# Kernel tuning notes

Measured on AMD Instinct MI355X. Metric: run time of the kernel, lower is better.

## Reference

```python
import jax, jax.numpy as jnp
import numpy as np
from jax import lax

K = 5        # kernel_size
KN = 32      # kernel_num
C_IN = 16
PRIOR_VAR = 0.01


def _extract_patches(x, k):
    # TF tf.image.extract_patches VALID, stride 1: last-dim order is (kh, kw, c)
    B, H, W, C = x.shape
    Ho, Wo = H - k + 1, W - k + 1
    p = jnp.stack([x[:, i:i + Ho, j:j + Wo, :] for i in range(k) for j in range(k)], axis=3)
    return p.reshape(B, Ho * Wo, k * k * C)  # [B, P, k*k*C]


def setup_inputs() -> dict:
    key = jax.random.key(0)
    k1, k2, k3, k4 = jax.random.split(key, 4)
    mu_in = jax.random.normal(k1, (32, 64, 64, C_IN), dtype=jnp.float32)
    Sigma_in = jax.random.uniform(k2, (32, 64, 64, C_IN), dtype=jnp.float32)
    # GlorotNormal for w_mu
    fan_in = K * K * C_IN
    fan_out = K * K * KN
    std = jnp.sqrt(2.0 / (fan_in + fan_out)).astype(jnp.float32)
    w_mu = jax.random.normal(k3, (K, K, C_IN, KN), dtype=jnp.float32) * std
    w_sigma = jax.random.uniform(k4, (KN,), dtype=jnp.float32, minval=-4.6, maxval=-2.25)
    return {"mu_in": mu_in, "Sigma_in": Sigma_in, "w_mu": w_mu, "w_sigma": w_sigma}


def reference(mu_in, Sigma_in, w_mu, w_sigma):
    B = mu_in.shape[0]
    # KL regularizer (broadcast w_sigma over w_mu shape, mean over all)
    kl_loss = (jnp.log(PRIOR_VAR) - 1.0 - w_sigma
               + jax.nn.softplus(w_sigma) / PRIOR_VAR
               + jnp.square(w_mu) / PRIOR_VAR)
    kl_conv = 0.5 * jnp.mean(kl_loss)

    w_sigma_2 = jax.nn.softplus(w_sigma)  # [KN]

    # mean path: standard conv
    mu_out = lax.conv_general_dilated(
        mu_in, w_mu, window_strides=(1, 1), padding='VALID',
        dimension_numbers=('NHWC', 'HWIO', 'NHWC'))  # [B, Ho, Wo, KN]
    Ho = mu_out.shape[1]

    mu_dim = jnp.float32(K * K * C_IN)

    diag_sigma_g = _extract_patches(Sigma_in, K)          # [B, P, D]
    mu_in_patches = _extract_patches(mu_in, K)            # [B, P, D]

    mu_cov_square = jnp.square(w_mu).reshape(K * K * C_IN, KN)
    mu_wT_sigmags_mu_w = diag_sigma_g @ (mu_cov_square / mu_dim)          # [B, P, KN]
    trace = jnp.sum(diag_sigma_g, axis=2, keepdims=True) * w_sigma_2 / mu_dim  # [B, P, KN]
    mu_gT_mu_g = jnp.sum(jnp.square(mu_in_patches), axis=-1, keepdims=True)    # [B, P, 1]
    sigmaw_mu_gT_mu_g = mu_gT_mu_g * w_sigma_2 / mu_dim                   # [B, P, KN]

    Sigma_out = trace + mu_wT_sigmags_mu_w + sigmaw_mu_gT_mu_g
    Sigma_out = jax.nn.softplus(Sigma_out.reshape(B, Ho, Ho, KN))
    return mu_out, Sigma_out, kl_conv
```

## Files before the change

kernel.cpp:

```cpp
#include <hip/hip_runtime.h>
#include <hip/hip_bf16.h>
#include <math.h>

#define KK 5
#define KN 32
#define CIN 16
#define H 64
#define W 64
#define NB 32
#define HO 60
#define WO 60
#define D_TOT 400
#define OUT_PLANE (NB*HO*WO*KN)

#define TH 8
#define TW 16
#define IN_R 12
#define IN_C 20
#define CPAD 24
#define TILE_SH (IN_R*IN_C*CPAD)
#define NKSTEP 13

typedef short short8 __attribute__((ext_vector_type(8)));
typedef float f32x4 __attribute__((ext_vector_type(4)));

__device__ ushort g_bmu[13312];
__device__ ushort g_bsq[13312];
__device__ float  g_spw[32];

__device__ __forceinline__ ushort f2bf(float x) {
    __hip_bfloat16 h = __float2bfloat16(x);
    return *reinterpret_cast<ushort*>(&h);
}
__device__ __forceinline__ float bf2f(ushort u) {
    __hip_bfloat16 h = *reinterpret_cast<__hip_bfloat16*>(&u);
    return __bfloat162float(h);
}
__device__ __forceinline__ float softplusf(float x) {
    return (x > 20.0f) ? x : __logf(1.0f + __expf(x));
}

__global__ void prep_all(const float* __restrict__ w_mu, const float* __restrict__ w_sigma,
                         float* __restrict__ kl_out) {
    __shared__ float red[256];
    int t = threadIdx.x;
    if (blockIdx.x < 52) {
        int idx = blockIdx.x * 256 + t;
        int j  = idx & 7;
        int l  = (idx >> 3) & 63;
        int nt = (idx >> 9) & 1;
        int ts = idx >> 10;
        int k  = ts * 32 + ((l >> 4) & 3) * 8 + j;
        int n  = nt * 16 + (l & 15);
        float w = (k < D_TOT) ? w_mu[k * KN + n] : 0.0f;
        g_bmu[idx] = f2bf(w);
        g_bsq[idx] = f2bf(w * w * (1.0f / 400.0f));
    } else {
        float s = 0.f;
        for (int i = t; i < D_TOT * KN; i += 256) { float w = w_mu[i]; s += w * w; }
        red[t] = s;
        __syncthreads();
        for (int off = 128; off > 0; off >>= 1) {
            if (t < off) red[t] += red[t + off];
            __syncthreads();
        }
        float sum_w2 = red[0];
        if (t < KN) {
            float ws = w_sigma[t];
            g_spw[t] = log1pf(expf(ws)) * (1.0f / 400.0f);
        }
        if (t == 0) {
            float sws = 0.f;
            for (int kn = 0; kn < KN; ++kn) {
                float ws = w_sigma[kn];
                float sp = log1pf(expf(ws));
                sws += -ws + sp * 100.0f;
            }
            float kl = 0.5f * (-4.605170186f - 1.0f + sws * (1.0f / 32.0f)
                               + sum_w2 * (100.0f / 12800.0f));
            *kl_out = kl;
        }
    }
}

__global__ __launch_bounds__(256, 4)
void vdp_main(const float* __restrict__ mu_in, const float* __restrict__ sig_in,
              float* __restrict__ mu_out, float* __restrict__ sig_out) {
    __shared__ ushort tiles[2 * TILE_SH + 8];
    __shared__ float csum[IN_R * IN_C];
    __shared__ float t12s[TH * TW];

    const int b   = blockIdx.z;
    const int ho0 = blockIdx.y * TH;
    const int wo0 = blockIdx.x * TW;
    const int t   = threadIdx.x;

    if (t < 8) tiles[2 * TILE_SH + t] = 0;

    for (int i = t; i < IN_R * IN_C * 4; i += 256) {
        int row = i / 80;
        int rem = i - row * 80;
        int col = rem >> 2, c4 = rem & 3;
        int gh = ho0 + row, gw = wo0 + col;
        float4 vm = make_float4(0.f, 0.f, 0.f, 0.f), vs = vm;
        if (gh < H && gw < W) {
            size_t g = (((size_t)b * H + gh) * W + gw) * CIN + c4 * 4;
            vm = *(const float4*)(mu_in + g);
            vs = *(const float4*)(sig_in + g);
        }
        int sb = (row * IN_C + col) * CPAD + c4 * 4;
        ushort4 um, us;
        um.x = f2bf(vm.x); um.y = f2bf(vm.y); um.z = f2bf(vm.z); um.w = f2bf(vm.w);
        us.x = f2bf(vs.x); us.y = f2bf(vs.y); us.z = f2bf(vs.z); us.w = f2bf(vs.w);
        *(ushort4*)&tiles[sb] = um;
        *(ushort4*)&tiles[TILE_SH + sb] = us;
    }
    __syncthreads();

    if (t < IN_R * IN_C) {
        int sb = t * CPAD;
        float acc = 0.f;
#pragma unroll
        for (int g = 0; g < 4; ++g) {
            ushort4 m4 = *(ushort4*)&tiles[sb + g * 4];
            ushort4 s4 = *(ushort4*)&tiles[TILE_SH + sb + g * 4];
            float m0 = bf2f(m4.x), m1 = bf2f(m4.y), m2 = bf2f(m4.z), m3 = bf2f(m4.w);
            acc += bf2f(s4.x) + bf2f(s4.y) + bf2f(s4.z) + bf2f(s4.w);
            acc += m0 * m0 + m1 * m1 + m2 * m2 + m3 * m3;
        }
        csum[t] = acc;
    }
    __syncthreads();

    if (t < TH * TW) {
        int r = t >> 4, c = t & 15;
        float s = 0.f;
#pragma unroll
        for (int kh = 0; kh < KK; ++kh)
#pragma unroll
            for (int kw = 0; kw < KK; ++kw)
                s += csum[(r + kh) * IN_C + c + kw];
        t12s[t] = s;
    }
    __syncthreads();

    const int w    = t >> 6;
    const int l    = t & 63;
    const int col  = l & 15;
    const int q    = l >> 4;
    const int qh   = q >> 1;
    const int qc   = q & 1;

    const char* lds = (const char*)tiles;
    int base0 = ((2 * w + 0) * IN_C + col) * (CPAD * 2) + qc * 16;
    int base1 = ((2 * w + 1) * IN_C + col) * (CPAD * 2) + qc * 16;
    const int qh48  = qh * 48;
    const int qh768 = qh * 768;
    const int zpad  = 2 * TILE_SH * 2;

    const short8* Bmu8 = (const short8*)g_bmu;
    const short8* Bsq8 = (const short8*)g_bsq;

    f32x4 accm[2][2], accs[2][2];
    f32x4 z = {0.f, 0.f, 0.f, 0.f};
#pragma unroll
    for (int a = 0; a < 2; ++a)
#pragma unroll
        for (int bn = 0; bn < 2; ++bn) { accm[a][bn] = z; accs[a][bn] = z; }

    constexpr int F0v[NKSTEP]  = {0, 2, 4, 21, 23, 40, 42, 44, 61, 63, 80, 82, 84};
    constexpr int D16[NKSTEP] = {0, 0, 1, 0, 0, 0, 0, 1, 0, 0, 0, 0, 2};

#pragma unroll
    for (int ts = 0; ts < NKSTEP; ++ts) {
        short8 am0, am1, as0, as1;
        if (D16[ts] == 2) {
            int a0 = qh ? zpad : (base0 + F0v[ts] * 48);
            int a1 = qh ? zpad : (base1 + F0v[ts] * 48);
            am0 = *(const short8*)(lds + a0);
            am1 = *(const short8*)(lds + a1);
            as0 = *(const short8*)(lds + a0 + (qh ? 0 : TILE_SH * 2));
            as1 = *(const short8*)(lds + a1 + (qh ? 0 : TILE_SH * 2));
        } else {
            int ex = (D16[ts] ? qh768 : qh48) + F0v[ts] * 48;
            am0 = *(const short8*)(lds + base0 + ex);
            am1 = *(const short8*)(lds + base1 + ex);
            as0 = *(const short8*)(lds + TILE_SH * 2 + base0 + ex);
            as1 = *(const short8*)(lds + TILE_SH * 2 + base1 + ex);
        }
        short8 bm0 = Bmu8[(ts * 2 + 0) * 64 + l];
        short8 bm1 = Bmu8[(ts * 2 + 1) * 64 + l];
        short8 bs0 = Bsq8[(ts * 2 + 0) * 64 + l];
        short8 bs1 = Bsq8[(ts * 2 + 1) * 64 + l];

        accm[0][0] = __builtin_amdgcn_mfma_f32_16x16x32_bf16(am0, bm0, accm[0][0], 0, 0, 0);
        accm[0][1] = __builtin_amdgcn_mfma_f32_16x16x32_bf16(am0, bm1, accm[0][1], 0, 0, 0);
        accm[1][0] = __builtin_amdgcn_mfma_f32_16x16x32_bf16(am1, bm0, accm[1][0], 0, 0, 0);
        accm[1][1] = __builtin_amdgcn_mfma_f32_16x16x32_bf16(am1, bm1, accm[1][1], 0, 0, 0);
        accs[0][0] = __builtin_amdgcn_mfma_f32_16x16x32_bf16(as0, bs0, accs[0][0], 0, 0, 0);
        accs[0][1] = __builtin_amdgcn_mfma_f32_16x16x32_bf16(as0, bs1, accs[0][1], 0, 0, 0);
        accs[1][0] = __builtin_amdgcn_mfma_f32_16x16x32_bf16(as1, bs0, accs[1][0], 0, 0, 0);
        accs[1][1] = __builtin_amdgcn_mfma_f32_16x16x32_bf16(as1, bs1, accs[1][1], 0, 0, 0);
    }

    float spw0 = g_spw[col], spw1 = g_spw[16 + col];
#pragma unroll
    for (int mt = 0; mt < 2; ++mt) {
        int ho = ho0 + 2 * w + mt;
        if (ho >= HO) continue;
#pragma unroll
        for (int reg = 0; reg < 4; ++reg) {
            int wo = wo0 + q * 4 + reg;
            if (wo >= WO) continue;
            float t12v = t12s[(2 * w + mt) * TW + q * 4 + reg];
            size_t base = (((size_t)b * HO + ho) * WO + wo) * KN;
            mu_out[base + col]      = accm[mt][0][reg];
            mu_out[base + 16 + col] = accm[mt][1][reg];
            float s0 = accs[mt][0][reg] + t12v * spw0;
            float s1 = accs[mt][1][reg] + t12v * spw1;
            sig_out[base + col]      = softplusf(s0);
            sig_out[base + 16 + col] = softplusf(s1);
        }
    }
}

extern "C" void kernel_launch(void* const* d_in, const int* in_sizes, int n_in,
                              void* d_out, int out_size, void* d_ws, size_t ws_size,
                              hipStream_t stream) {
    const float* mu_in   = (const float*)d_in[0];
    const float* sig_in  = (const float*)d_in[1];
    const float* w_mu    = (const float*)d_in[2];
    const float* w_sigma = (const float*)d_in[3];

    float* out     = (float*)d_out;
    float* mu_out  = out;
    float* sig_out = out + (size_t)OUT_PLANE;
    float* kl_out  = out + 2 * (size_t)OUT_PLANE;

    (void)d_ws; (void)ws_size;

    prep_all<<<53, 256, 0, stream>>>(w_mu, w_sigma, kl_out);
    vdp_main<<<dim3(4, 8, NB), 256, 0, stream>>>(mu_in, sig_in, mu_out, sig_out);
}
```

Before: 113.5 us.

## Switch conv MFMA to 32x32x16 per kernel position and fuse row-sum reduction

Replaces the 16x16x32 MFMA tiling, whose K steps crossed kernel positions and needed zero padding, with one 32x32x16 MFMA per (kh,kw) position covering all 16 input channels and all 32 output channels. Weight prep is rearranged to match. This removes the padding steps and the irregular address tables. The per-pixel channel sum is now computed from fp32 values with lane shuffles during the tile load, which drops one LDS pass and one barrier. The epilogue also changes: each lane writes a single output channel across 16 rows, so store patterns and the register footprint are different.

```diff
diff --git a/kernel.cpp b/kernel.cpp
--- a/kernel.cpp
+++ b/kernel.cpp
@@ -19,22 +19,18 @@
 #define IN_C 20
 #define CPAD 24
 #define TILE_SH (IN_R*IN_C*CPAD)
-#define NKSTEP 13
+#define NPOS 25
 
 typedef short short8 __attribute__((ext_vector_type(8)));
-typedef float f32x4 __attribute__((ext_vector_type(4)));
+typedef float f32x16 __attribute__((ext_vector_type(16)));
 
-__device__ ushort g_bmu[13312];
-__device__ ushort g_bsq[13312];
-__device__ float  g_spw[32];
+__device__ ushort g_bmu[NPOS * 64 * 8];
+__device__ ushort g_bsq[NPOS * 64 * 8];
+__device__ float  g_spw[KN];
 
 __device__ __forceinline__ ushort f2bf(float x) {
     __hip_bfloat16 h = __float2bfloat16(x);
     return *reinterpret_cast<ushort*>(&h);
-}
-__device__ __forceinline__ float bf2f(ushort u) {
-    __hip_bfloat16 h = *reinterpret_cast<__hip_bfloat16*>(&u);
-    return __bfloat162float(h);
 }
 __device__ __forceinline__ float softplusf(float x) {
     return (x > 20.0f) ? x : __logf(1.0f + __expf(x));
@@ -44,15 +40,14 @@
                          float* __restrict__ kl_out) {
     __shared__ float red[256];
     int t = threadIdx.x;
-    if (blockIdx.x < 52) {
+    if (blockIdx.x < 50) {
         int idx = blockIdx.x * 256 + t;
         int j  = idx & 7;
         int l  = (idx >> 3) & 63;
-        int nt = (idx >> 9) & 1;
-        int ts = idx >> 10;
-        int k  = ts * 32 + ((l >> 4) & 3) * 8 + j;
-        int n  = nt * 16 + (l & 15);
-        float w = (k < D_TOT) ? w_mu[k * KN + n] : 0.0f;
+        int ts = idx >> 9;
+        int cin = ((l >> 5) & 1) * 8 + j;
+        int n   = l & 31;
+        float w = w_mu[ts * 512 + cin * 32 + n];
         g_bmu[idx] = f2bf(w);
         g_bsq[idx] = f2bf(w * w * (1.0f / 400.0f));
     } else {
@@ -86,7 +81,7 @@
 __global__ __launch_bounds__(256, 4)
 void vdp_main(const float* __restrict__ mu_in, const float* __restrict__ sig_in,
               float* __restrict__ mu_out, float* __restrict__ sig_out) {
-    __shared__ ushort tiles[2 * TILE_SH + 8];
+    __shared__ ushort tiles[2 * TILE_SH];
     __shared__ float csum[IN_R * IN_C];
     __shared__ float t12s[TH * TW];
 
@@ -95,12 +90,10 @@
     const int wo0 = blockIdx.x * TW;
     const int t   = threadIdx.x;
 
-    if (t < 8) tiles[2 * TILE_SH + t] = 0;
-
     for (int i = t; i < IN_R * IN_C * 4; i += 256) {
-        int row = i / 80;
-        int rem = i - row * 80;
-        int col = rem >> 2, c4 = rem & 3;
+        int pix = i >> 2, c4 = i & 3;
+        int row = pix / IN_C;
+        int col = pix - row * IN_C;
         int gh = ho0 + row, gw = wo0 + col;
         float4 vm = make_float4(0.f, 0.f, 0.f, 0.f), vs = vm;
         if (gh < H && gw < W) {
@@ -108,27 +101,17 @@
             vm = *(const float4*)(mu_in + g);
             vs = *(const float4*)(sig_in + g);
         }
-        int sb = (row * IN_C + col) * CPAD + c4 * 4;
+        int sb = pix * CPAD + c4 * 4;
         ushort4 um, us;
         um.x = f2bf(vm.x); um.y = f2bf(vm.y); um.z = f2bf(vm.z); um.w = f2bf(vm.w);
         us.x = f2bf(vs.x); us.y = f2bf(vs.y); us.z = f2bf(vs.z); us.w = f2bf(vs.w);
         *(ushort4*)&tiles[sb] = um;
         *(ushort4*)&tiles[TILE_SH + sb] = us;
-    }
-    __syncthreads();
-
-    if (t < IN_R * IN_C) {
-        int sb = t * CPAD;
-        float acc = 0.f;
-#pragma unroll
-        for (int g = 0; g < 4; ++g) {
-            ushort4 m4 = *(ushort4*)&tiles[sb + g * 4];
-            ushort4 s4 = *(ushort4*)&tiles[TILE_SH + sb + g * 4];
-            float m0 = bf2f(m4.x), m1 = bf2f(m4.y), m2 = bf2f(m4.z), m3 = bf2f(m4.w);
-            acc += bf2f(s4.x) + bf2f(s4.y) + bf2f(s4.z) + bf2f(s4.w);
-            acc += m0 * m0 + m1 * m1 + m2 * m2 + m3 * m3;
-        }
-        csum[t] = acc;
+        float part = vs.x + vs.y + vs.z + vs.w
+                   + vm.x * vm.x + vm.y * vm.y + vm.z * vm.z + vm.w * vm.w;
+        part += __shfl_down(part, 2, 4);
+        part += __shfl_down(part, 1, 4);
+        if (c4 == 0) csum[pix] = part;
     }
     __syncthreads();
 
@@ -144,82 +127,48 @@
     }
     __syncthreads();
 
-    const int w    = t >> 6;
-    const int l    = t & 63;
-    const int col  = l & 15;
-    const int q    = l >> 4;
-    const int qh   = q >> 1;
-    const int qc   = q & 1;
+    const int w   = t >> 6;
+    const int l   = t & 63;
+    const int p   = l & 31;
+    const int hi  = l >> 5;
+    const int pr  = p >> 4;
+    const int pc  = p & 15;
 
     const char* lds = (const char*)tiles;
-    int base0 = ((2 * w + 0) * IN_C + col) * (CPAD * 2) + qc * 16;
-    int base1 = ((2 * w + 1) * IN_C + col) * (CPAD * 2) + qc * 16;
-    const int qh48  = qh * 48;
-    const int qh768 = qh * 768;
-    const int zpad  = 2 * TILE_SH * 2;
+    const int abase = ((2 * w + pr) * IN_C + pc) * (CPAD * 2) + hi * 16;
 
     const short8* Bmu8 = (const short8*)g_bmu;
     const short8* Bsq8 = (const short8*)g_bsq;
 
-    f32x4 accm[2][2], accs[2][2];
-    f32x4 z = {0.f, 0.f, 0.f, 0.f};
+    f32x16 accm = {0.f}, accs = {0.f};
 #pragma unroll
-    for (int a = 0; a < 2; ++a)
+    for (int kh = 0; kh < KK; ++kh) {
 #pragma unroll
-        for (int bn = 0; bn < 2; ++bn) { accm[a][bn] = z; accs[a][bn] = z; }
-
-    constexpr int F0v[NKSTEP]  = {0, 2, 4, 21, 23, 40, 42, 44, 61, 63, 80, 82, 84};
-    constexpr int D16[NKSTEP] = {0, 0, 1, 0, 0, 0, 0, 1, 0, 0, 0, 0, 2};
-
-#pragma unroll
-    for (int ts = 0; ts < NKSTEP; ++ts) {
-        short8 am0, am1, as0, as1;
-        if (D16[ts] == 2) {
-            int a0 = qh ? zpad : (base0 + F0v[ts] * 48);
-            int a1 = qh ? zpad : (base1 + F0v[ts] * 48);
-            am0 = *(const short8*)(lds + a0);
-            am1 = *(const short8*)(lds + a1);
-            as0 = *(const short8*)(lds + a0 + (qh ? 0 : TILE_SH * 2));
-            as1 = *(const short8*)(lds + a1 + (qh ? 0 : TILE_SH * 2));
-        } else {
-            int ex = (D16[ts] ? qh768 : qh48) + F0v[ts] * 48;
-            am0 = *(const short8*)(lds + base0 + ex);
-            am1 = *(const short8*)(lds + base1 + ex);
-            as0 = *(const short8*)(lds + TILE_SH * 2 + base0 + ex);
-            as1 = *(const short8*)(lds + TILE_SH * 2 + base1 + ex);
+        for (int kw = 0; kw < KK; ++kw) {
+            const int ts  = kh * KK + kw;
+            const int off = (kh * IN_C + kw) * (CPAD * 2);
+            short8 am = *(const short8*)(lds + abase + off);
+            short8 as = *(const short8*)(lds + abase + off + TILE_SH * 2);
+            short8 bm = Bmu8[ts * 64 + l];
+            short8 bs = Bsq8[ts * 64 + l];
+            accm = __builtin_amdgcn_mfma_f32_32x32x16_bf16(am, bm, accm, 0, 0, 0);
+            accs = __builtin_amdgcn_mfma_f32_32x32x16_bf16(as, bs, accs, 0, 0, 0);
         }
-        short8 bm0 = Bmu8[(ts * 2 + 0) * 64 + l];
-        short8 bm1 = Bmu8[(ts * 2 + 1) * 64 + l];
-        short8 bs0 = Bsq8[(ts * 2 + 0) * 64 + l];
-        short8 bs1 = Bsq8[(ts * 2 + 1) * 64 + l];
-
-        accm[0][0] = __builtin_amdgcn_mfma_f32_16x16x32_bf16(am0, bm0, accm[0][0], 0, 0, 0);
-        accm[0][1] = __builtin_amdgcn_mfma_f32_16x16x32_bf16(am0, bm1, accm[0][1], 0, 0, 0);
-        accm[1][0] = __builtin_amdgcn_mfma_f32_16x16x32_bf16(am1, bm0, accm[1][0], 0, 0, 0);
-        accm[1][1] = __builtin_amdgcn_mfma_f32_16x16x32_bf16(am1, bm1, accm[1][1], 0, 0, 0);
-        accs[0][0] = __builtin_amdgcn_mfma_f32_16x16x32_bf16(as0, bs0, accs[0][0], 0, 0, 0);
-        accs[0][1] = __builtin_amdgcn_mfma_f32_16x16x32_bf16(as0, bs1, accs[0][1], 0, 0, 0);
-        accs[1][0] = __builtin_amdgcn_mfma_f32_16x16x32_bf16(as1, bs0, accs[1][0], 0, 0, 0);
-        accs[1][1] = __builtin_amdgcn_mfma_f32_16x16x32_bf16(as1, bs1, accs[1][1], 0, 0, 0);
     }
 
-    float spw0 = g_spw[col], spw1 = g_spw[16 + col];
+    const int n = l & 31;
+    const float spwn = g_spw[n];
 #pragma unroll
-    for (int mt = 0; mt < 2; ++mt) {
-        int ho = ho0 + 2 * w + mt;
-        if (ho >= HO) continue;
-#pragma unroll
-        for (int reg = 0; reg < 4; ++reg) {
-            int wo = wo0 + q * 4 + reg;
-            if (wo >= WO) continue;
-            float t12v = t12s[(2 * w + mt) * TW + q * 4 + reg];
-            size_t base = (((size_t)b * HO + ho) * WO + wo) * KN;
-            mu_out[base + col]      = accm[mt][0][reg];
-            mu_out[base + 16 + col] = accm[mt][1][reg];
-            float s0 = accs[mt][0][reg] + t12v * spw0;
-            float s1 = accs[mt][1][reg] + t12v * spw1;
-            sig_out[base + col]      = softplusf(s0);
-            sig_out[base + 16 + col] = softplusf(s1);
+    for (int reg = 0; reg < 16; ++reg) {
+        int rloc = (reg & 3) + 8 * (reg >> 2) + 4 * hi;
+        int lr = rloc >> 4, lc = rloc & 15;
+        int ho = ho0 + 2 * w + lr;
+        int wo = wo0 + lc;
+        if (ho < HO && wo < WO) {
+            float t12v = t12s[(2 * w + lr) * TW + lc];
+            size_t base = (((size_t)b * HO + ho) * WO + wo) * KN + n;
+            mu_out[base]  = accm[reg];
+            sig_out[base] = softplusf(accs[reg] + t12v * spwn);
         }
     }
 }
@@ -239,6 +188,6 @@
 
     (void)d_ws; (void)ws_size;
 
-    prep_all<<<53, 256, 0, stream>>>(w_mu, w_sigma, kl_out);
+    prep_all<<<51, 256, 0, stream>>>(w_mu, w_sigma, kl_out);
     vdp_main<<<dim3(4, 8, NB), 256, 0, stream>>>(mu_in, sig_in, mu_out, sig_out);
 }
```

After: 114.1 us (median of 2 runs). About the same (+0.5%).
